# Kernel optimization log

Hardware: AMD Instinct MI355X
Metric: run time of the kernel (lower is better)

Reference implementation:

```python
import jax, jax.numpy as jnp
import numpy as np

B = 16384
D = 20          # input_size == hidden_size
L = 1000        # num_layers (all hidden layers, uniform 20x20)


def setup_inputs() -> dict:
    key = jax.random.key(0)
    kx, kw, kb, kwo, kbo = jax.random.split(key, 5)
    scale = 1.0 / np.sqrt(D)
    x = jax.random.normal(kx, (B, D), dtype=jnp.float32)
    # 1000 stacked Linear(20,20) layers; torch Linear weight is (out, in)
    W = jax.random.normal(kw, (L, D, D), dtype=jnp.float32) * scale
    b = jax.random.normal(kb, (L, D), dtype=jnp.float32) * scale
    # final Linear(20, 1)
    W_out = jax.random.normal(kwo, (1, D), dtype=jnp.float32) * scale
    b_out = jax.random.normal(kbo, (1,), dtype=jnp.float32) * scale
    return {"x": x, "W": W, "b": b, "W_out": W_out, "b_out": b_out}


def reference(x, W, b, W_out, b_out):
    def step(h, wb):
        w, bb = wb  # w: [D, D] (out, in), bb: [D]
        h = jax.nn.sigmoid(h @ w.T + bb)  # [B, D]
        return h, None

    h, _ = jax.lax.scan(step, x, (W, b))
    # final Linear(D, 1) + sigmoid
    out = jax.nn.sigmoid(h @ W_out.T + b_out)  # [B, 1]
    return out
```

## Files before the change

### kernel.cpp

```cpp
#include <hip/hip_runtime.h>

#define LOG2E 1.44269504088896340736f

typedef __attribute__((ext_vector_type(8))) short short8;
typedef __attribute__((ext_vector_type(4))) float f32x4;

constexpr int CL       = 10;
constexpr int LAYER_BY = 2048;
constexpr int CHUNK_BY = CL * LAYER_BY;
constexpr int CHUNK_V4 = CHUNK_BY / 16;
constexpr int V4_PER_T = CHUNK_V4 / 256;

__device__ __forceinline__ int slot_pos(int h, int e) {
    return (e < 4) ? (4 * h + e) : (16 + 4 * h + (e - 4));
}

__device__ __forceinline__ unsigned short f32_to_bf16_rne(float f) {
    unsigned u = __builtin_bit_cast(unsigned, f);
    unsigned r = 0x7fffu + ((u >> 16) & 1u);
    return (unsigned short)((u + r) >> 16);
}

__global__ void prepack(const float* __restrict__ W, const float* __restrict__ b,
                        unsigned int* __restrict__ wstream, int L)
{
    const int l    = blockIdx.x;
    const int t    = threadIdx.x >> 6;
    const int lane = threadIdx.x & 63;
    const int n    = t * 16 + (lane & 15);
    const int h    = lane >> 4;
    unsigned int words[4];
#pragma unroll
    for (int d = 0; d < 4; ++d) {
        unsigned short halves[2];
#pragma unroll
        for (int half = 0; half < 2; ++half) {
            int e   = d * 2 + half;
            int pos = slot_pos(h, e);
            float v = 0.f;
            if (n < 20) {
                if (pos < 20)       v = W[(size_t)l * 400 + n * 20 + pos];
                else if (pos == 20) v = b[(size_t)l * 20 + n];
            }
            halves[half] = f32_to_bf16_rne(v);
        }
        words[d] = (unsigned)halves[0] | ((unsigned)halves[1] << 16);
    }
    unsigned int* dst = wstream + ((size_t)l * LAYER_BY + t * 1024 + lane * 16) / 4;
    dst[0] = words[0]; dst[1] = words[1]; dst[2] = words[2]; dst[3] = words[3];
}

__device__ __forceinline__ unsigned cvt_pk_bf16(float lo, float hi) {
    unsigned r;
    asm("v_cvt_pk_bf16_f32 %0, %1, %2" : "=v"(r) : "v"(lo), "v"(hi));
    return r;
}

__device__ __forceinline__ short8 finalize_B(unsigned p0, unsigned p1,
                                             unsigned p2, unsigned p3, int h) {
    if (h != 0) { p2 = (h == 1) ? 0x00003F80u : 0u; p3 = 0u; }
    union { unsigned u[4]; short8 s; } cv;
    cv.u[0] = p0; cv.u[1] = p1; cv.u[2] = p2; cv.u[3] = p3;
    return cv.s;
}

__device__ __forceinline__ float sigm(float z) {
    return __builtin_amdgcn_rcpf(1.f + __builtin_amdgcn_exp2f(-LOG2E * z));
}

__global__ __launch_bounds__(256, 1) void mann_mfma(
    const float* __restrict__ x, const unsigned int* __restrict__ wstream,
    const float* __restrict__ Wout, const float* __restrict__ bout,
    float* __restrict__ out, int B, int L)
{
    __shared__ unsigned char lds[2 * CHUNK_BY];

    const int tid  = threadIdx.x;
    const int lane = tid & 63;
    const int c16  = lane & 15;
    const int h    = lane >> 4;
    const int w    = (blockIdx.x * 256 + tid) >> 6;
    const int row  = w * 16 + c16;

    const float4 xa = *reinterpret_cast<const float4*>(x + (size_t)row * 20 + 4 * h);
    const float4 xb = *reinterpret_cast<const float4*>(x + (size_t)row * 20 + 16);
    short8 Bf = finalize_B(cvt_pk_bf16(xa.x, xa.y), cvt_pk_bf16(xa.z, xa.w),
                           cvt_pk_bf16(xb.x, xb.y), cvt_pk_bf16(xb.z, xb.w), h);

    float4 sreg[V4_PER_T];
    auto stage_load = [&](int c) {
        const float4* g = reinterpret_cast<const float4*>(wstream) + (size_t)c * CHUNK_V4;
#pragma unroll
        for (int j = 0; j < V4_PER_T; ++j) sreg[j] = g[j * 256 + tid];
    };
    auto stage_write = [&](int bufi) {
        float4* d = reinterpret_cast<float4*>(lds + bufi * CHUNK_BY);
#pragma unroll
        for (int j = 0; j < V4_PER_T; ++j) d[j * 256 + tid] = sreg[j];
    };

    const unsigned lbase = (unsigned)(uintptr_t)&lds[0];

    stage_load(0); stage_write(0); __syncthreads();

    short8 a0A, a1A, a0B, a1B;
    auto issue_A = [&](unsigned addr, short8& t0, short8& t1) {
        asm volatile("ds_read_b128 %0, %1 offset:0"    : "=v"(t0) : "v"(addr));
        asm volatile("ds_read_b128 %0, %1 offset:1024" : "=v"(t1) : "v"(addr));
    };
    issue_A(lbase + lane * 16, a0A, a1A);

    const f32x4 zero = {0.f, 0.f, 0.f, 0.f};
    float s0, s1, s2, s3, s4, s5, s6, s7;

    const int NC = L / CL;
    for (int c = 0; c < NC; ++c) {
        if (c + 1 < NC) stage_load(c + 1);
        const unsigned cb = lbase + (c & 1) * CHUNK_BY + lane * 16;
#pragma unroll
        for (int ll = 0; ll < CL; ++ll) {
            const bool even = (ll & 1) == 0;
            short8& c0 = even ? a0A : a0B;
            short8& c1 = even ? a1A : a1B;
            short8& n0 = even ? a0B : a0A;
            short8& n1 = even ? a1B : a1A;
            asm volatile("s_waitcnt lgkmcnt(0)" ::: "memory");
            __builtin_amdgcn_sched_barrier(0);
            if (ll + 1 < CL) issue_A(cb + (ll + 1) * LAYER_BY, n0, n1);
            f32x4 acc0 = __builtin_amdgcn_mfma_f32_16x16x32_bf16(c0, Bf, zero, 0, 0, 0);
            f32x4 acc1 = __builtin_amdgcn_mfma_f32_16x16x32_bf16(c1, Bf, zero, 0, 0, 0);
            s0 = sigm(acc0[0]); s1 = sigm(acc0[1]); s2 = sigm(acc0[2]); s3 = sigm(acc0[3]);
            s4 = sigm(acc1[0]); s5 = sigm(acc1[1]); s6 = sigm(acc1[2]); s7 = sigm(acc1[3]);
            Bf = finalize_B(cvt_pk_bf16(s0, s1), cvt_pk_bf16(s2, s3),
                            cvt_pk_bf16(s4, s5), cvt_pk_bf16(s6, s7), h);
        }
        if (c + 1 < NC) {
            stage_write((c + 1) & 1);
            __syncthreads();
            issue_A(lbase + ((c + 1) & 1) * CHUNK_BY + lane * 16, a0A, a1A);
        }
    }

    const float4 woa = *reinterpret_cast<const float4*>(Wout + 4 * h);
    const float4 wob = *reinterpret_cast<const float4*>(Wout + 16);
    float part = s0 * woa.x + s1 * woa.y + s2 * woa.z + s3 * woa.w;
    const float m = (h == 0) ? 1.f : 0.f;
    part += m * (s4 * wob.x + s5 * wob.y + s6 * wob.z + s7 * wob.w);
    part += __shfl_xor(part, 16, 64);
    part += __shfl_xor(part, 32, 64);
    if (h == 0) out[row] = sigm(part + bout[0]);
}

extern "C" void kernel_launch(void* const* d_in, const int* in_sizes, int n_in,
                              void* d_out, int out_size, void* d_ws, size_t ws_size,
                              hipStream_t stream) {
    const float* x    = (const float*)d_in[0];
    const float* W    = (const float*)d_in[1];
    const float* b    = (const float*)d_in[2];
    const float* Wout = (const float*)d_in[3];
    const float* bout = (const float*)d_in[4];
    float* out = (float*)d_out;

    const int B = in_sizes[0] / 20;
    const int L = in_sizes[1] / 400;

    unsigned int* wstream = (unsigned int*)d_ws;

    prepack<<<L, 128, 0, stream>>>(W, b, wstream, L);

    const int grid = B / 64;
    mann_mfma<<<grid, 256, 0, stream>>>(x, wstream, Wout, bout, out, B, L);
}
```

Baseline: 273.3 us.

## Switch to fp16 16x16x16 MFMAs with Padé tanh sigmoid and deeper LDS prefetch

New measurement: 254.0 us (median of 2 runs). 1.08x faster.

```diff
diff --git a/kernel.cpp b/kernel.cpp
--- a/kernel.cpp
+++ b/kernel.cpp
@@ -2,70 +2,110 @@
 
 #define LOG2E 1.44269504088896340736f
 
-typedef __attribute__((ext_vector_type(8))) short short8;
+typedef __attribute__((ext_vector_type(8))) _Float16 half8;
+typedef __attribute__((ext_vector_type(4))) _Float16 half4;
 typedef __attribute__((ext_vector_type(4))) float f32x4;
-
-constexpr int CL       = 10;
-constexpr int LAYER_BY = 2048;
+typedef __attribute__((ext_vector_type(2))) float f32x2;
+typedef __attribute__((ext_vector_type(2))) unsigned int uint2v;
+
+constexpr int CL       = 8;
+constexpr int LAYER_BY = 1536;
 constexpr int CHUNK_BY = CL * LAYER_BY;
 constexpr int CHUNK_V4 = CHUNK_BY / 16;
 constexpr int V4_PER_T = CHUNK_V4 / 256;
 
-__device__ __forceinline__ int slot_pos(int h, int e) {
-    return (e < 4) ? (4 * h + e) : (16 + 4 * h + (e - 4));
-}
-
-__device__ __forceinline__ unsigned short f32_to_bf16_rne(float f) {
-    unsigned u = __builtin_bit_cast(unsigned, f);
-    unsigned r = 0x7fffu + ((u >> 16) & 1u);
-    return (unsigned short)((u + r) >> 16);
+
+__device__ __forceinline__ unsigned short f16_rne(float f) {
+    _Float16 h = (_Float16)f;
+    return __builtin_bit_cast(unsigned short, h);
 }
 
 __global__ void prepack(const float* __restrict__ W, const float* __restrict__ b,
                         unsigned int* __restrict__ wstream, int L)
 {
     const int l    = blockIdx.x;
-    const int t    = threadIdx.x >> 6;
-    const int lane = threadIdx.x & 63;
-    const int n    = t * 16 + (lane & 15);
+    const int lane = threadIdx.x;
+    const int n    = lane & 15;
     const int h    = lane >> 4;
-    unsigned int words[4];
-#pragma unroll
-    for (int d = 0; d < 4; ++d) {
-        unsigned short halves[2];
-#pragma unroll
-        for (int half = 0; half < 2; ++half) {
-            int e   = d * 2 + half;
-            int pos = slot_pos(h, e);
-            float v = 0.f;
-            if (n < 20) {
-                if (pos < 20)       v = W[(size_t)l * 400 + n * 20 + pos];
-                else if (pos == 20) v = b[(size_t)l * 20 + n];
-            }
-            halves[half] = f32_to_bf16_rne(v);
+
+    unsigned short v[12];
+#pragma unroll
+    for (int e = 0; e < 4; ++e) {
+        v[e] = f16_rne(0.5f * W[(size_t)l * 400 + n * 20 + (4 * h + e)]);
+        int p = 16 + 4 * h + e;
+        float a = 0.f;
+        if (p < 20)       a = 0.5f * W[(size_t)l * 400 + n * 20 + p];
+        else if (p == 20) a = 0.5f * b[(size_t)l * 20 + n];
+        v[4 + e] = f16_rne(a);
+        float c = 0.f;
+        int m1 = 16 + n;
+        if (m1 < 20) {
+            if (p < 20)       c = 0.5f * W[(size_t)l * 400 + m1 * 20 + p];
+            else if (p == 20) c = 0.5f * b[(size_t)l * 20 + m1];
         }
-        words[d] = (unsigned)halves[0] | ((unsigned)halves[1] << 16);
+        v[8 + e] = f16_rne(c);
     }
-    unsigned int* dst = wstream + ((size_t)l * LAYER_BY + t * 1024 + lane * 16) / 4;
-    dst[0] = words[0]; dst[1] = words[1]; dst[2] = words[2]; dst[3] = words[3];
-}
-
-__device__ __forceinline__ unsigned cvt_pk_bf16(float lo, float hi) {
-    unsigned r;
-    asm("v_cvt_pk_bf16_f32 %0, %1, %2" : "=v"(r) : "v"(lo), "v"(hi));
-    return r;
-}
-
-__device__ __forceinline__ short8 finalize_B(unsigned p0, unsigned p1,
-                                             unsigned p2, unsigned p3, int h) {
-    if (h != 0) { p2 = (h == 1) ? 0x00003F80u : 0u; p3 = 0u; }
-    union { unsigned u[4]; short8 s; } cv;
-    cv.u[0] = p0; cv.u[1] = p1; cv.u[2] = p2; cv.u[3] = p3;
-    return cv.s;
+    unsigned w0 = (unsigned)v[0] | ((unsigned)v[1]  << 16);
+    unsigned w1 = (unsigned)v[2] | ((unsigned)v[3]  << 16);
+    unsigned w2 = (unsigned)v[4] | ((unsigned)v[5]  << 16);
+    unsigned w3 = (unsigned)v[6] | ((unsigned)v[7]  << 16);
+    unsigned w4 = (unsigned)v[8] | ((unsigned)v[9]  << 16);
+    unsigned w5 = (unsigned)v[10]| ((unsigned)v[11] << 16);
+
+    unsigned int* d0 = wstream + ((size_t)l * LAYER_BY + lane * 16) / 4;
+    d0[0] = w0; d0[1] = w1; d0[2] = w2; d0[3] = w3;
+    unsigned int* d1 = wstream + ((size_t)l * LAYER_BY + 1024 + lane * 8) / 4;
+    d1[0] = w4; d1[1] = w5;
+}
+
+__device__ __forceinline__ unsigned pkrtz(float a, float b) {
+    auto r = __builtin_amdgcn_cvt_pkrtz(a, b);
+    return __builtin_bit_cast(unsigned, r);
+}
+__device__ __forceinline__ half4 mk_half4(unsigned lo, unsigned hi) {
+    uint2v u; u.x = lo; u.y = hi;
+    return __builtin_bit_cast(half4, u);
+}
+
+__device__ __forceinline__ f32x2 make2(float v) { f32x2 r; r.x = v; r.y = v; return r; }
+
+__device__ __forceinline__ f32x2 pade_sig(f32x2 x) {
+    f32x2 u = x * x;
+    f32x2 n = (u * make2(0.5f) + make2(52.5f)) * u + make2(472.5f);
+    f32x2 d = (u * make2(15.0f) + make2(420.0f)) * u + make2(945.0f);
+    float pr = __builtin_amdgcn_rcpf(d.x * d.y);
+    f32x2 inv; inv.x = pr * d.y; inv.y = pr * d.x;
+    return (x * n) * inv + make2(0.5f);
 }
 
 __device__ __forceinline__ float sigm(float z) {
     return __builtin_amdgcn_rcpf(1.f + __builtin_amdgcn_exp2f(-LOG2E * z));
+}
+
+#define ISSUE_FRAG(base1, base2, OFF, A0, A1)                                   \
+    asm volatile("ds_read_b128 %0, %1 offset:" #OFF : "=v"(A0) : "v"(base1));   \
+    asm volatile("ds_read_b64 %0, %1 offset:" #OFF : "=v"(A1) : "v"(base2));
+
+__device__ __forceinline__ void layer_step(const half8& a0, const half4& a1,
+                                           half4& Bk0, half4& Bk1,
+                                           f32x2 (&q)[4], int h) {
+    const f32x4 z4 = {0.f, 0.f, 0.f, 0.f};
+    const half4 A0k0 = __builtin_shufflevector(a0, a0, 0, 1, 2, 3);
+    const half4 A0k1 = __builtin_shufflevector(a0, a0, 4, 5, 6, 7);
+    f32x4 acc1 = __builtin_amdgcn_mfma_f32_16x16x16f16(a1,   Bk1, z4, 0, 0, 0);
+    f32x4 acc0 = __builtin_amdgcn_mfma_f32_16x16x16f16(A0k0, Bk0, z4, 0, 0, 0);
+    acc0       = __builtin_amdgcn_mfma_f32_16x16x16f16(A0k1, Bk1, acc0, 0, 0, 0);
+    q[2].x = acc1[0]; q[2].y = acc1[1];
+    q[3].x = acc1[2]; q[3].y = acc1[3];
+    q[2] = pade_sig(q[2]); q[3] = pade_sig(q[3]);
+    q[0].x = acc0[0]; q[0].y = acc0[1];
+    q[1].x = acc0[2]; q[1].y = acc0[3];
+    q[0] = pade_sig(q[0]); q[1] = pade_sig(q[1]);
+    Bk0 = mk_half4(pkrtz(q[0].x, q[0].y), pkrtz(q[1].x, q[1].y));
+    unsigned k1w0 = (h == 0) ? pkrtz(q[2].x, q[2].y)
+                             : ((h == 1) ? 0x00003C00u : 0u);
+    unsigned k1w1 = (h == 0) ? pkrtz(q[3].x, q[3].y) : 0u;
+    Bk1 = mk_half4(k1w0, k1w1);
 }
 
 __global__ __launch_bounds__(256, 1) void mann_mfma(
@@ -84,8 +124,10 @@
 
     const float4 xa = *reinterpret_cast<const float4*>(x + (size_t)row * 20 + 4 * h);
     const float4 xb = *reinterpret_cast<const float4*>(x + (size_t)row * 20 + 16);
-    short8 Bf = finalize_B(cvt_pk_bf16(xa.x, xa.y), cvt_pk_bf16(xa.z, xa.w),
-                           cvt_pk_bf16(xb.x, xb.y), cvt_pk_bf16(xb.z, xb.w), h);
+    half4 Bk0 = mk_half4(pkrtz(xa.x, xa.y), pkrtz(xa.z, xa.w));
+    unsigned iw0 = (h == 0) ? pkrtz(xb.x, xb.y) : ((h == 1) ? 0x00003C00u : 0u);
+    unsigned iw1 = (h == 0) ? pkrtz(xb.z, xb.w) : 0u;
+    half4 Bk1 = mk_half4(iw0, iw1);
 
     float4 sreg[V4_PER_T];
     auto stage_load = [&](int c) {
@@ -100,52 +142,62 @@
     };
 
     const unsigned lbase = (unsigned)(uintptr_t)&lds[0];
+    const unsigned b1A = lbase + lane * 16;
+    const unsigned b2A = lbase + 1024 + lane * 8;
+    const unsigned b1B = b1A + CHUNK_BY;
+    const unsigned b2B = b2A + CHUNK_BY;
 
     stage_load(0); stage_write(0); __syncthreads();
 
-    short8 a0A, a1A, a0B, a1B;
-    auto issue_A = [&](unsigned addr, short8& t0, short8& t1) {
-        asm volatile("ds_read_b128 %0, %1 offset:0"    : "=v"(t0) : "v"(addr));
-        asm volatile("ds_read_b128 %0, %1 offset:1024" : "=v"(t1) : "v"(addr));
-    };
-    issue_A(lbase + lane * 16, a0A, a1A);
-
-    const f32x4 zero = {0.f, 0.f, 0.f, 0.f};
-    float s0, s1, s2, s3, s4, s5, s6, s7;
+    half8 f0a, f1a, f2a, f3a;
+    half4 f0b, f1b, f2b, f3b;
+
+    ISSUE_FRAG(b1A, b2A, 0,    f0a, f0b);
+    ISSUE_FRAG(b1A, b2A, 1536, f1a, f1b);
+
+    f32x2 q[4];
 
     const int NC = L / CL;
     for (int c = 0; c < NC; ++c) {
         if (c + 1 < NC) stage_load(c + 1);
-        const unsigned cb = lbase + (c & 1) * CHUNK_BY + lane * 16;
+        const unsigned cb1 = (c & 1) ? b1B : b1A;
+        const unsigned cb2 = (c & 1) ? b2B : b2A;
 #pragma unroll
         for (int ll = 0; ll < CL; ++ll) {
-            const bool even = (ll & 1) == 0;
-            short8& c0 = even ? a0A : a0B;
-            short8& c1 = even ? a1A : a1B;
-            short8& n0 = even ? a0B : a0A;
-            short8& n1 = even ? a1B : a1A;
-            asm volatile("s_waitcnt lgkmcnt(0)" ::: "memory");
+            if (ll == CL - 1) asm volatile("s_waitcnt lgkmcnt(0)");
+            else              asm volatile("s_waitcnt lgkmcnt(2)");
             __builtin_amdgcn_sched_barrier(0);
-            if (ll + 1 < CL) issue_A(cb + (ll + 1) * LAYER_BY, n0, n1);
-            f32x4 acc0 = __builtin_amdgcn_mfma_f32_16x16x32_bf16(c0, Bf, zero, 0, 0, 0);
-            f32x4 acc1 = __builtin_amdgcn_mfma_f32_16x16x32_bf16(c1, Bf, zero, 0, 0, 0);
-            s0 = sigm(acc0[0]); s1 = sigm(acc0[1]); s2 = sigm(acc0[2]); s3 = sigm(acc0[3]);
-            s4 = sigm(acc1[0]); s5 = sigm(acc1[1]); s6 = sigm(acc1[2]); s7 = sigm(acc1[3]);
-            Bf = finalize_B(cvt_pk_bf16(s0, s1), cvt_pk_bf16(s2, s3),
-                            cvt_pk_bf16(s4, s5), cvt_pk_bf16(s6, s7), h);
+            switch (ll + 2 < CL ? (ll + 2) : -1) {
+                case 2: ISSUE_FRAG(cb1, cb2, 3072,  f2a, f2b); break;
+                case 3: ISSUE_FRAG(cb1, cb2, 4608,  f3a, f3b); break;
+                case 4: ISSUE_FRAG(cb1, cb2, 6144,  f0a, f0b); break;
+                case 5: ISSUE_FRAG(cb1, cb2, 7680,  f1a, f1b); break;
+                case 6: ISSUE_FRAG(cb1, cb2, 9216,  f2a, f2b); break;
+                case 7: ISSUE_FRAG(cb1, cb2, 10752, f3a, f3b); break;
+                default: break;
+            }
+            __builtin_amdgcn_sched_barrier(0);
+            const int ci = ll & 3;
+            if      (ci == 0) layer_step(f0a, f0b, Bk0, Bk1, q, h);
+            else if (ci == 1) layer_step(f1a, f1b, Bk0, Bk1, q, h);
+            else if (ci == 2) layer_step(f2a, f2b, Bk0, Bk1, q, h);
+            else              layer_step(f3a, f3b, Bk0, Bk1, q, h);
         }
         if (c + 1 < NC) {
             stage_write((c + 1) & 1);
             __syncthreads();
-            issue_A(lbase + ((c + 1) & 1) * CHUNK_BY + lane * 16, a0A, a1A);
+            const unsigned nb1 = ((c + 1) & 1) ? b1B : b1A;
+            const unsigned nb2 = ((c + 1) & 1) ? b2B : b2A;
+            ISSUE_FRAG(nb1, nb2, 0,    f0a, f0b);
+            ISSUE_FRAG(nb1, nb2, 1536, f1a, f1b);
         }
     }
 
     const float4 woa = *reinterpret_cast<const float4*>(Wout + 4 * h);
     const float4 wob = *reinterpret_cast<const float4*>(Wout + 16);
-    float part = s0 * woa.x + s1 * woa.y + s2 * woa.z + s3 * woa.w;
+    float part = q[0].x * woa.x + q[0].y * woa.y + q[1].x * woa.z + q[1].y * woa.w;
     const float m = (h == 0) ? 1.f : 0.f;
-    part += m * (s4 * wob.x + s5 * wob.y + s6 * wob.z + s7 * wob.w);
+    part += m * (q[2].x * wob.x + q[2].y * wob.y + q[3].x * wob.z + q[3].y * wob.w);
     part += __shfl_xor(part, 16, 64);
     part += __shfl_xor(part, 32, 64);
     if (h == 0) out[row] = sigm(part + bout[0]);
@@ -166,7 +218,7 @@
 
     unsigned int* wstream = (unsigned int*)d_ws;
 
-    prepack<<<L, 128, 0, stream>>>(W, b, wstream, L);
+    prepack<<<L, 64, 0, stream>>>(W, b, wstream, L);
 
     const int grid = B / 64;
     mann_mfma<<<grid, 256, 0, stream>>>(x, wstream, Wout, bout, out, B, L);
```
